# Kernel tuning notes

Measured on AMD Instinct MI355X. Metric: run time of the kernel, lower is better.

Reference implementation:

```python
import jax, jax.numpy as jnp
import numpy as np
import math

EMBED_DIM = 64

def setup_inputs() -> dict:
    key = jax.random.key(0)
    ks = jax.random.split(key, 9)
    B, S, H, E = 2, 2048, 8, EMBED_DIM
    f16 = jnp.float16
    inp = {
        'query': jax.random.normal(ks[0], (B, S, H, E), dtype=f16),
        'key':   jax.random.normal(ks[1], (B, S, H, E), dtype=f16),
        'value': jax.random.normal(ks[2], (B, S, H, E), dtype=f16),
        # Linear params (torch Linear: y = x @ W.T + b); W stored as [out,in]
        'Wq': (jax.random.normal(ks[3], (E, E), dtype=f16) / np.float16(math.sqrt(E))),
        'bq': jax.random.normal(ks[4], (E,), dtype=f16) * np.float16(0.02),
        'Wk': (jax.random.normal(ks[5], (E, E), dtype=f16) / np.float16(math.sqrt(E))),
        'bk': jax.random.normal(ks[6], (E,), dtype=f16) * np.float16(0.02),
        'Wv': (jax.random.normal(ks[7], (E, E), dtype=f16) / np.float16(math.sqrt(E))),
        'bv': jax.random.normal(ks[8], (E,), dtype=f16) * np.float16(0.02),
    }
    return inp

def reference(query, key, value, Wq, bq, Wk, bk, Wv, bv):
    # Linear projections on last dim, fused with permute(0,2,1,3): [B,S,H,E] -> [B,H,S,E]
    q = jnp.einsum('bshe,fe->bhsf', query, Wq) + bq
    k = jnp.einsum('bshe,fe->bhsf', key, Wk) + bk
    v = jnp.einsum('bshe,fe->bhsf', value, Wv) + bv
    scale = jnp.asarray(1.0 / math.sqrt(q.shape[-1]), dtype=q.dtype)
    q = q * scale
    # full attention matrix [B,H,S,S], fp16 matmul then fp32 softmax (faithful to source)
    scores = jnp.einsum('bhse,bhte->bhst', q, k).astype(jnp.float32)
    attn = jax.nn.softmax(scores, axis=-1).astype(jnp.float16)
    out = jnp.einsum('bhst,bhte->bhse', attn, v)
    return out
```

## Files before the change

kernel.cpp:

```cpp
#include <hip/hip_runtime.h>

#define S_LEN 2048
#define NH    8
#define EMB   64
#define BM    128
#define BN    64
#define NKT   (S_LEN / BN)
#define NSPLIT 3
#define PSTR  72
#define M_INIT  (-1.0e4f)
#define EXP_CLAMP (-80.0f)

typedef _Float16 half8   __attribute__((ext_vector_type(8)));
typedef _Float16 half4   __attribute__((ext_vector_type(4)));
typedef float    float4_t __attribute__((ext_vector_type(4)));
typedef float    float8_t __attribute__((ext_vector_type(8)));

__device__ inline half8 cvt8(const float* p) {
    float8_t f = *reinterpret_cast<const float8_t*>(p);
    half8 h;
    #pragma unroll
    for (int j = 0; j < 8; ++j) h[j] = (_Float16)f[j];
    return h;
}

__device__ inline void gload_lds16(const _Float16* g, _Float16* l) {
    __builtin_amdgcn_global_load_lds(
        (const __attribute__((address_space(1))) void*)g,
        (__attribute__((address_space(3))) void*)l, 16, 0, 0);
}

__global__ __launch_bounds__(256) void proj_seg(
    const float* __restrict__ q_in, const float* __restrict__ k_in,
    const float* __restrict__ v_in,
    const float* __restrict__ Wq, const float* __restrict__ bq,
    const float* __restrict__ Wk, const float* __restrict__ bk,
    const float* __restrict__ Wv, const float* __restrict__ bv_,
    float* __restrict__ Qout, _Float16* __restrict__ KT8,
    _Float16* __restrict__ VT8, int segBase)
{
    const int seg = segBase + (blockIdx.x >> 8);
    const int bid = blockIdx.x & 255;
    const float* X    = (seg == 0) ? q_in : (seg == 1) ? k_in : v_in;
    const float* W    = (seg == 0) ? Wq   : (seg == 1) ? Wk   : Wv;
    const float* bias = (seg == 0) ? bq   : (seg == 1) ? bk   : bv_;

    const int tid  = threadIdx.x;
    const int lane = tid & 63;
    const int wave = tid >> 6;
    const int l15  = lane & 15;
    const int quad = lane >> 4;
    const int gwave = bid * 4 + wave;

    half8 wf[4][2];
    #pragma unroll
    for (int ft = 0; ft < 4; ++ft)
        #pragma unroll
        for (int ks = 0; ks < 2; ++ks)
            wf[ft][ks] = cvt8(W + (ft * 16 + l15) * 64 + ks * 32 + quad * 8);
    float bv[4];
    #pragma unroll
    for (int ft = 0; ft < 4; ++ft) bv[ft] = bias[ft * 16 + l15];

    #pragma unroll
    for (int rt2 = 0; rt2 < 2; ++rt2) {
        const int rt = gwave * 2 + rt2;
        const int arow = rt * 16 + l15;
        half8 xf[2];
        #pragma unroll
        for (int ks = 0; ks < 2; ++ks)
            xf[ks] = cvt8(X + (long)arow * 64 + ks * 32 + quad * 8);
        float4_t acc[4];
        #pragma unroll
        for (int ft = 0; ft < 4; ++ft) {
            acc[ft] = (float4_t){0.f, 0.f, 0.f, 0.f};
            #pragma unroll
            for (int ks = 0; ks < 2; ++ks)
                acc[ft] = __builtin_amdgcn_mfma_f32_16x16x32_f16(
                    xf[ks], wf[ft][ks], acc[ft], 0, 0, 0);
        }
        #pragma unroll
        for (int r = 0; r < 4; ++r) {
            const int row = rt * 16 + quad * 4 + r;
            const int b = row >> 14;
            const int s = (row >> 3) & 2047;
            const int h = row & 7;
            const int bh = b * NH + h;
            #pragma unroll
            for (int ft = 0; ft < 4; ++ft) {
                const _Float16 v = (_Float16)(acc[ft][r] + bv[ft]);
                const int f = ft * 16 + l15;
                if (seg == 0)
                    Qout[((long)bh * S_LEN + s) * EMB + f] =
                        (float)(v * (_Float16)0.125f);
                else if (seg == 1)
                    KT8[(((long)bh * 8 + (f >> 3)) * S_LEN + s) * 8 + (f & 7)] = v;
                else
                    VT8[(((long)bh * 256 + (s >> 3)) * 64 + f) * 8 + (s & 7)] = v;
            }
        }
    }
}

__global__ __launch_bounds__(256, 3) void attn_part(
    const _Float16* __restrict__ KT, const _Float16* __restrict__ VT,
    const float* __restrict__ Qbuf,
    _Float16* __restrict__ p0, _Float16* __restrict__ p1,
    _Float16* __restrict__ p2, float* __restrict__ stats)
{
    __shared__ __align__(16) _Float16 Kb[8 * 64 * 8];
    __shared__ __align__(16) _Float16 Vb[8 * 64 * 8];
    __shared__ __align__(16) _Float16 Pl[4][32 * PSTR];

    const int tid  = threadIdx.x;
    const int lane = tid & 63;
    const int wave = tid >> 6;
    const int l15  = lane & 15;
    const int quad = lane >> 4;
    const int bx   = blockIdx.x;
    const int bh   = bx / (16 * NSPLIT);
    const int rem  = bx % (16 * NSPLIT);
    const int qt   = rem / NSPLIT;
    const int sp   = rem % NSPLIT;
    const long base = (long)bh * S_LEN * EMB;
    const int qrow0 = qt * BM + wave * 32;

    const _Float16* kg = KT + (long)bh * 8 * S_LEN * 8;

    half8 qf[2][2];
    #pragma unroll
    for (int g = 0; g < 2; ++g)
        #pragma unroll
        for (int ks = 0; ks < 2; ++ks)
            qf[g][ks] = cvt8(Qbuf + base + (long)(qrow0 + g * 16 + l15) * EMB
                             + ks * 32 + quad * 8);

    float4_t o[2][4];
    #pragma unroll
    for (int g = 0; g < 2; ++g)
        #pragma unroll
        for (int et = 0; et < 4; ++et) o[g][et] = (float4_t){0.f, 0.f, 0.f, 0.f};
    float m_run[2] = {M_INIT, M_INIT}, l_run[2] = {0.f, 0.f};

    const int kb = (sp * NKT) / NSPLIT, ke = ((sp + 1) * NKT) / NSPLIT;
    for (int kt = kb; kt < ke; ++kt) {
        if (kt > kb) __syncthreads();
        const int t0 = kt * BN;
        #pragma unroll
        for (int rr = 0; rr < 2; ++rr) {
            const int u = rr * 256 + tid;
            const int ec = u >> 6, tl = u & 63;
            gload_lds16(kg + ((long)ec * S_LEN + t0 + tl) * 8, Kb + u * 8);
        }
        const _Float16* vg = VT + ((long)bh * 256 + (t0 >> 3)) * 512;
        #pragma unroll
        for (int rr = 0; rr < 2; ++rr) {
            const int u = rr * 256 + tid;
            gload_lds16(vg + u * 8, Vb + u * 8);
        }
        __syncthreads();

        float4_t sacc[2][4];
        #pragma unroll
        for (int g = 0; g < 2; ++g)
            #pragma unroll
            for (int nt = 0; nt < 4; ++nt)
                sacc[g][nt] = (float4_t){0.f, 0.f, 0.f, 0.f};
        #pragma unroll
        for (int nt = 0; nt < 4; ++nt)
            #pragma unroll
            for (int ks = 0; ks < 2; ++ks) {
                half8 kf = *reinterpret_cast<const half8*>(
                    Kb + (ks * 4 + quad) * 512 + (nt * 16 + l15) * 8);
                sacc[0][nt] = __builtin_amdgcn_mfma_f32_16x16x32_f16(
                    kf, qf[0][ks], sacc[0][nt], 0, 0, 0);
                sacc[1][nt] = __builtin_amdgcn_mfma_f32_16x16x32_f16(
                    kf, qf[1][ks], sacc[1][nt], 0, 0, 0);
            }

        _Float16* Pw = Pl[wave];
        #pragma unroll
        for (int g = 0; g < 2; ++g) {
            float mx = sacc[g][0][0];
            #pragma unroll
            for (int nt = 0; nt < 4; ++nt)
                #pragma unroll
                for (int r = 0; r < 4; ++r) mx = fmaxf(mx, sacc[g][nt][r]);
            mx = fmaxf(mx, __shfl_xor(mx, 16));
            mx = fmaxf(mx, __shfl_xor(mx, 32));
            const float mn = fmaxf(m_run[g], mx);
            const float alpha = __expf(fmaxf(m_run[g] - mn, EXP_CLAMP));
            m_run[g] = mn;
            float rsum = 0.f;
            #pragma unroll
            for (int nt = 0; nt < 4; ++nt) {
                half4 ph;
                #pragma unroll
                for (int r = 0; r < 4; ++r) {
                    const float p = __expf(sacc[g][nt][r] - m_run[g]);
                    rsum += p;
                    ph[r] = (_Float16)p;
                }
                *reinterpret_cast<half4*>(
                    &Pw[(g * 16 + l15) * PSTR + nt * 16 + quad * 4]) = ph;
            }
            rsum += __shfl_xor(rsum, 16);
            rsum += __shfl_xor(rsum, 32);
            l_run[g] = l_run[g] * alpha + rsum;
            #pragma unroll
            for (int r = 0; r < 4; ++r) {
                const float ar = __shfl(alpha, quad * 4 + r);
                #pragma unroll
                for (int et = 0; et < 4; ++et) o[g][et][r] *= ar;
            }
        }

        #pragma unroll
        for (int ts = 0; ts < 2; ++ts) {
            half8 vfr[4];
            #pragma unroll
            for (int et = 0; et < 4; ++et)
                vfr[et] = *reinterpret_cast<const half8*>(
                    Vb + (ts * 4 + quad) * 512 + (et * 16 + l15) * 8);
            #pragma unroll
            for (int g = 0; g < 2; ++g) {
                half8 pf = *reinterpret_cast<const half8*>(
                    &Pw[(g * 16 + l15) * PSTR + ts * 32 + quad * 8]);
                #pragma unroll
                for (int et = 0; et < 4; ++et)
                    o[g][et] = __builtin_amdgcn_mfma_f32_16x16x32_f16(
                        pf, vfr[et], o[g][et], 0, 0, 0);
            }
        }
    }

    _Float16* pp = (sp == 0) ? p0 : (sp == 1) ? p1 : p2;
    #pragma unroll
    for (int g = 0; g < 2; ++g)
        #pragma unroll
        for (int r = 0; r < 4; ++r) {
            const float lr = __shfl(l_run[g], quad * 4 + r);
            const float inv = 1.f / lr;
            const int row = qrow0 + g * 16 + quad * 4 + r;
            const int R = bh * S_LEN + row;
            #pragma unroll
            for (int et = 0; et < 4; ++et)
                pp[(long)R * EMB + et * 16 + l15] = (_Float16)(o[g][et][r] * inv);
        }
    if (lane < 16) {
        #pragma unroll
        for (int g = 0; g < 2; ++g) {
            const int R = bh * S_LEN + qrow0 + g * 16 + lane;
            stats[sp * 32768 + R] = m_run[g];
            stats[(NSPLIT + sp) * 32768 + R] = l_run[g];
        }
    }
}

__global__ __launch_bounds__(256) void attn_combine(
    const _Float16* __restrict__ p0, const _Float16* __restrict__ p1,
    const _Float16* __restrict__ p2, const float* __restrict__ stats,
    float* __restrict__ out)
{
    const int gid = blockIdx.x * 256 + threadIdx.x;
    const int R  = gid >> 2;
    const int c0 = (gid & 3) * 16;
    const float m0 = stats[R], m1 = stats[32768 + R], m2 = stats[2 * 32768 + R];
    const float l0 = stats[3 * 32768 + R], l1 = stats[4 * 32768 + R],
                l2 = stats[5 * 32768 + R];
    const float M = fmaxf(fmaxf(m0, m1), m2);
    float w0 = l0 * __expf(fmaxf(m0 - M, EXP_CLAMP));
    float w1 = l1 * __expf(fmaxf(m1 - M, EXP_CLAMP));
    float w2 = l2 * __expf(fmaxf(m2 - M, EXP_CLAMP));
    const float rinv = 1.f / (w0 + w1 + w2);
    w0 *= rinv; w1 *= rinv; w2 *= rinv;
    const long i0 = (long)R * EMB + c0;
    #pragma unroll
    for (int h = 0; h < 2; ++h) {
        half8 a = *reinterpret_cast<const half8*>(p0 + i0 + h * 8);
        half8 b = *reinterpret_cast<const half8*>(p1 + i0 + h * 8);
        half8 c = *reinterpret_cast<const half8*>(p2 + i0 + h * 8);
        #pragma unroll
        for (int j = 0; j < 8; ++j)
            out[i0 + h * 8 + j] = (float)(_Float16)(
                w0 * (float)a[j] + w1 * (float)b[j] + w2 * (float)c[j]);
    }
}

extern "C" void kernel_launch(void* const* d_in, const int* in_sizes, int n_in,
                              void* d_out, int out_size, void* d_ws, size_t ws_size,
                              hipStream_t stream) {
    const float* q_in = (const float*)d_in[0];
    const float* k_in = (const float*)d_in[1];
    const float* v_in = (const float*)d_in[2];
    const float* Wq   = (const float*)d_in[3];
    const float* bq   = (const float*)d_in[4];
    const float* Wk   = (const float*)d_in[5];
    const float* bk   = (const float*)d_in[6];
    const float* Wv   = (const float*)d_in[7];
    const float* bv   = (const float*)d_in[8];
    float* out = (float*)d_out;

    _Float16* KT8   = (_Float16*)d_in[0];
    _Float16* VT8   = (_Float16*)((char*)d_in[0] + (4u << 20));
    _Float16* part0 = (_Float16*)d_in[2];
    _Float16* part1 = part0 + (long)2 * 1024 * 1024;
    _Float16* part2 = (_Float16*)d_in[1];
    float*    stats = (float*)((char*)d_in[1] + (4u << 20));

    proj_seg<<<256, 256, 0, stream>>>(q_in, k_in, v_in, Wq, bq, Wk, bk,
                                      Wv, bv, out, KT8, VT8, 0);
    proj_seg<<<512, 256, 0, stream>>>(q_in, k_in, v_in, Wq, bq, Wk, bk,
                                      Wv, bv, out, KT8, VT8, 1);
    attn_part<<<16 * 16 * NSPLIT, 256, 0, stream>>>(KT8, VT8, out,
                                                    part0, part1, part2, stats);
    attn_combine<<<512, 256, 0, stream>>>(part0, part1, part2, stats, out);
}
```

Measured before the change: 142.0 us.

## Use exp2 with log2e-folded Q scale and compute row sums via MFMA

Folds log2(e) into the Q scaling so the softmax can use exp2f instead of __expf, saving a multiply per element. It also drops the scalar row-sum and its cross-lane shuffles, and instead accumulates the softmax denominator with an extra MFMA of P against a vector of ones. The sums are now taken from the fp16-rounded P, which matches the values used for P·V. The cost is one extra MFMA per P fragment and slightly different rounding, since Q is now scaled in fp32 rather than fp16.

```diff
diff --git a/kernel.cpp b/kernel.cpp
--- a/kernel.cpp
+++ b/kernel.cpp
@@ -10,6 +10,7 @@
 #define PSTR  72
 #define M_INIT  (-1.0e4f)
 #define EXP_CLAMP (-80.0f)
+#define QSCALE  (0.125f * 1.4426950408889634f)
 
 typedef _Float16 half8   __attribute__((ext_vector_type(8)));
 typedef _Float16 half4   __attribute__((ext_vector_type(4)));
@@ -91,8 +92,7 @@
                 const _Float16 v = (_Float16)(acc[ft][r] + bv[ft]);
                 const int f = ft * 16 + l15;
                 if (seg == 0)
-                    Qout[((long)bh * S_LEN + s) * EMB + f] =
-                        (float)(v * (_Float16)0.125f);
+                    Qout[((long)bh * S_LEN + s) * EMB + f] = (float)v * QSCALE;
                 else if (seg == 1)
                     KT8[(((long)bh * 8 + (f >> 3)) * S_LEN + s) * 8 + (f & 7)] = v;
                 else
@@ -135,12 +135,18 @@
             qf[g][ks] = cvt8(Qbuf + base + (long)(qrow0 + g * 16 + l15) * EMB
                              + ks * 32 + quad * 8);
 
-    float4_t o[2][4];
-    #pragma unroll
-    for (int g = 0; g < 2; ++g)
+    half8 ones;
+    #pragma unroll
+    for (int j = 0; j < 8; ++j) ones[j] = (_Float16)1.0f;
+
+    float4_t o[2][4], lq[2];
+    #pragma unroll
+    for (int g = 0; g < 2; ++g) {
+        lq[g] = (float4_t){0.f, 0.f, 0.f, 0.f};
         #pragma unroll
         for (int et = 0; et < 4; ++et) o[g][et] = (float4_t){0.f, 0.f, 0.f, 0.f};
-    float m_run[2] = {M_INIT, M_INIT}, l_run[2] = {0.f, 0.f};
+    }
+    float m_run[2] = {M_INIT, M_INIT};
 
     const int kb = (sp * NKT) / NSPLIT, ke = ((sp + 1) * NKT) / NSPLIT;
     for (int kt = kb; kt < ke; ++kt) {
@@ -189,29 +195,23 @@
             mx = fmaxf(mx, __shfl_xor(mx, 16));
             mx = fmaxf(mx, __shfl_xor(mx, 32));
             const float mn = fmaxf(m_run[g], mx);
-            const float alpha = __expf(fmaxf(m_run[g] - mn, EXP_CLAMP));
+            const float alpha = exp2f(fmaxf(m_run[g] - mn, EXP_CLAMP));
             m_run[g] = mn;
-            float rsum = 0.f;
             #pragma unroll
             for (int nt = 0; nt < 4; ++nt) {
                 half4 ph;
                 #pragma unroll
-                for (int r = 0; r < 4; ++r) {
-                    const float p = __expf(sacc[g][nt][r] - m_run[g]);
-                    rsum += p;
-                    ph[r] = (_Float16)p;
-                }
+                for (int r = 0; r < 4; ++r)
+                    ph[r] = (_Float16)exp2f(sacc[g][nt][r] - mn);
                 *reinterpret_cast<half4*>(
                     &Pw[(g * 16 + l15) * PSTR + nt * 16 + quad * 4]) = ph;
             }
-            rsum += __shfl_xor(rsum, 16);
-            rsum += __shfl_xor(rsum, 32);
-            l_run[g] = l_run[g] * alpha + rsum;
             #pragma unroll
             for (int r = 0; r < 4; ++r) {
                 const float ar = __shfl(alpha, quad * 4 + r);
                 #pragma unroll
                 for (int et = 0; et < 4; ++et) o[g][et][r] *= ar;
+                lq[g][r] *= ar;
             }
         }
 
@@ -226,6 +226,8 @@
             for (int g = 0; g < 2; ++g) {
                 half8 pf = *reinterpret_cast<const half8*>(
                     &Pw[(g * 16 + l15) * PSTR + ts * 32 + quad * 8]);
+                lq[g] = __builtin_amdgcn_mfma_f32_16x16x32_f16(
+                    pf, ones, lq[g], 0, 0, 0);
                 #pragma unroll
                 for (int et = 0; et < 4; ++et)
                     o[g][et] = __builtin_amdgcn_mfma_f32_16x16x32_f16(
@@ -239,8 +241,7 @@
     for (int g = 0; g < 2; ++g)
         #pragma unroll
         for (int r = 0; r < 4; ++r) {
-            const float lr = __shfl(l_run[g], quad * 4 + r);
-            const float inv = 1.f / lr;
+            const float inv = 1.f / lq[g][r];
             const int row = qrow0 + g * 16 + quad * 4 + r;
             const int R = bh * S_LEN + row;
             #pragma unroll
@@ -252,8 +253,16 @@
         for (int g = 0; g < 2; ++g) {
             const int R = bh * S_LEN + qrow0 + g * 16 + lane;
             stats[sp * 32768 + R] = m_run[g];
-            stats[(NSPLIT + sp) * 32768 + R] = l_run[g];
-        }
+        }
+    }
+    if (l15 == 0) {
+        #pragma unroll
+        for (int g = 0; g < 2; ++g)
+            #pragma unroll
+            for (int r = 0; r < 4; ++r) {
+                const int R = bh * S_LEN + qrow0 + g * 16 + quad * 4 + r;
+                stats[(NSPLIT + sp) * 32768 + R] = lq[g][r];
+            }
     }
 }
 
@@ -269,9 +278,9 @@
     const float l0 = stats[3 * 32768 + R], l1 = stats[4 * 32768 + R],
                 l2 = stats[5 * 32768 + R];
     const float M = fmaxf(fmaxf(m0, m1), m2);
-    float w0 = l0 * __expf(fmaxf(m0 - M, EXP_CLAMP));
-    float w1 = l1 * __expf(fmaxf(m1 - M, EXP_CLAMP));
-    float w2 = l2 * __expf(fmaxf(m2 - M, EXP_CLAMP));
+    float w0 = l0 * exp2f(fmaxf(m0 - M, EXP_CLAMP));
+    float w1 = l1 * exp2f(fmaxf(m1 - M, EXP_CLAMP));
+    float w2 = l2 * exp2f(fmaxf(m2 - M, EXP_CLAMP));
     const float rinv = 1.f / (w0 + w1 + w2);
     w0 *= rinv; w1 *= rinv; w2 *= rinv;
     const long i0 = (long)R * EMB + c0;
```

Result: slower. 145.4 us (+2.4%).
